# Performance work log

Measured on AMD Instinct MI355X. Metric: run time of the kernel, lower is better.

The kernel has to match this reference:

```python
import jax, jax.numpy as jnp
import numpy as np

DIM = 768
HEADS = 12
HEAD_DIM = DIM // HEADS
HIDDEN = 4 * DIM
EPS = 1e-5


def layernorm(x, g, b):
    mu = jnp.mean(x, axis=-1, keepdims=True)
    var = jnp.var(x, axis=-1, keepdims=True)
    return (x - mu) * jax.lax.rsqrt(var + EPS) * g + b


def setup_inputs() -> dict:
    key = jax.random.key(0)
    ks = jax.random.split(key, 16)
    s = 0.02
    return {
        "x_pre": jax.random.normal(ks[0], (8, 512, DIM), jnp.float32),
        "x_post": jax.random.normal(ks[1], (8, 512, DIM), jnp.float32),
        "attention_mask": jnp.zeros((8, 1, 1024, 1024), jnp.float32),
        "ln1_g": jnp.ones((DIM,), jnp.float32),
        "ln1_b": jnp.zeros((DIM,), jnp.float32),
        "Wq": jax.random.normal(ks[2], (DIM, DIM), jnp.float32) * s,
        "bq": jnp.zeros((DIM,), jnp.float32),
        "Wk": jax.random.normal(ks[3], (DIM, DIM), jnp.float32) * s,
        "bk": jnp.zeros((DIM,), jnp.float32),
        "Wv": jax.random.normal(ks[4], (DIM, DIM), jnp.float32) * s,
        "bv": jnp.zeros((DIM,), jnp.float32),
        "Wo": jax.random.normal(ks[5], (DIM, DIM), jnp.float32) * s,
        "bo": jnp.zeros((DIM,), jnp.float32),
        "ln2_g": jnp.ones((DIM,), jnp.float32),
        "ln2_b": jnp.zeros((DIM,), jnp.float32),
        "W1": jax.random.normal(ks[6], (DIM, HIDDEN), jnp.float32) * s,
        "b1": jnp.zeros((HIDDEN,), jnp.float32),
        "W2": jax.random.normal(ks[7], (HIDDEN, DIM), jnp.float32) * s,
        "b2": jnp.zeros((DIM,), jnp.float32),
        "gamma_1": 0.1 * jnp.ones((DIM,), jnp.float32),
        "gamma_2": 0.1 * jnp.ones((DIM,), jnp.float32),
    }


def reference(x_pre, x_post, attention_mask, ln1_g, ln1_b, Wq, bq, Wk, bk, Wv, bv,
              Wo, bo, ln2_g, ln2_b, W1, b1, W2, b2, gamma_1, gamma_2):
    x = jnp.concatenate((x_pre, x_post), axis=1)  # [B, N, C]
    B, N, C = x.shape
    h = layernorm(x, ln1_g, ln1_b)
    # self-attention with manual QK^T in float32
    q = (h @ Wq + bq).reshape(B, N, HEADS, HEAD_DIM)
    k = (h @ Wk + bk).reshape(B, N, HEADS, HEAD_DIM)
    v = (h @ Wv + bv).reshape(B, N, HEADS, HEAD_DIM)
    scale = HEAD_DIM ** -0.5
    attn = jnp.einsum("bqhd,bkhd->bhqk", q.astype(jnp.float32) * scale,
                      k.astype(jnp.float32)) + attention_mask
    attn = jax.nn.softmax(attn, axis=-1).astype(x.dtype)
    o = jnp.einsum("bhqk,bkhd->bqhd", attn, v).reshape(B, N, C)
    o = o @ Wo + bo
    x = x + gamma_1 * o
    # MLP
    h2 = layernorm(x, ln2_g, ln2_b)
    h2 = jax.nn.gelu(h2 @ W1 + b1, approximate=False) @ W2 + b2
    return x + gamma_2 * h2
```

## Files before the change

kernel.cpp:

```cpp
#include <hip/hip_runtime.h>
#include <hip/hip_fp8.h>
#include <cstdint>
#include <cstddef>

#define BATCH   8
#define SEQ     1024
#define DIMC    768
#define HEADS   12
#define HDIM    64
#define HIDDEN  3072
#define MROWS   (BATCH * SEQ)
#define L2E     1.4426950408889634f

typedef __attribute__((ext_vector_type(8))) short bf16x8;
typedef __attribute__((ext_vector_type(4))) float f32x4;

__device__ __forceinline__ unsigned short f2b(float f) {
    union { float f; unsigned int u; } v; v.f = f;
    unsigned int u = v.u;
    return (unsigned short)((u + 0x7FFFu + ((u >> 16) & 1u)) >> 16);
}
__device__ __forceinline__ unsigned char f2e4m3(float f) {
    __hip_fp8_e4m3 t(f); return t.__x;
}
__device__ __forceinline__ unsigned int b2u(float f) {
    union { float f; unsigned int u; } v; v.f = f; return v.u;
}
__device__ __forceinline__ float u2f(unsigned int u) {
    union { unsigned int u; float f; } v; v.u = u; return v.f;
}
__device__ __forceinline__ unsigned int pack2(float a, float b) {
    return ((b2u(a) + 0x8000u) >> 16) | (((b2u(b) + 0x8000u) & 0xFFFF0000u));
}
__device__ __forceinline__ void gl_lds16(const void* g, void* l) {
    __builtin_amdgcn_global_load_lds(
        (const __attribute__((address_space(1))) unsigned int*)g,
        (__attribute__((address_space(3))) unsigned int*)l, 16, 0, 0);
}
__device__ __forceinline__ float gelu_fast(float x) {
    float p = x * x;
    float a = fmaf(p, 0.044715f, 1.0f);
    float w = x * a * -2.302118131f;
    float z = exp2f(w);
    return x * __builtin_amdgcn_rcpf(1.0f + z);
}

__global__ __launch_bounds__(256) void tcvt_k(const float* __restrict__ src,
                                              unsigned char* __restrict__ dst,
                                              int K, int N) {
    __shared__ float tile[32][33];
    int k0 = blockIdx.y * 32, n0 = blockIdx.x * 32;
    int tx = threadIdx.x, ty = threadIdx.y;
#pragma unroll
    for (int i = 0; i < 4; i++)
        tile[ty + i * 8][tx] = src[(size_t)(k0 + ty + i * 8) * N + n0 + tx];
    __syncthreads();
#pragma unroll
    for (int i = 0; i < 4; i++)
        dst[(size_t)(n0 + ty + i * 8) * K + k0 + tx] = f2e4m3(tile[tx][ty + i * 8]);
}

__global__ __launch_bounds__(256) void tcvt4_k(const float* __restrict__ s0,
                                               const float* __restrict__ s1,
                                               const float* __restrict__ s2,
                                               const float* __restrict__ s3,
                                               unsigned char* __restrict__ d0,
                                               unsigned char* __restrict__ d1,
                                               unsigned char* __restrict__ d2,
                                               unsigned char* __restrict__ d3) {
    const float* src = (blockIdx.z == 0) ? s0 : (blockIdx.z == 1) ? s1
                     : (blockIdx.z == 2) ? s2 : s3;
    unsigned char* dst = (blockIdx.z == 0) ? d0 : (blockIdx.z == 1) ? d1
                       : (blockIdx.z == 2) ? d2 : d3;
    __shared__ float tile[32][33];
    int k0 = blockIdx.y * 32, n0 = blockIdx.x * 32;
    int tx = threadIdx.x, ty = threadIdx.y;
#pragma unroll
    for (int i = 0; i < 4; i++)
        tile[ty + i * 8][tx] = src[(size_t)(k0 + ty + i * 8) * DIMC + n0 + tx];
    __syncthreads();
#pragma unroll
    for (int i = 0; i < 4; i++)
        dst[(size_t)(n0 + ty + i * 8) * DIMC + k0 + tx] = f2e4m3(tile[tx][ty + i * 8]);
}

__global__ __launch_bounds__(256) void mprep_k(const float* __restrict__ m,
                                               unsigned short* __restrict__ mb) {
    size_t i = ((size_t)blockIdx.x * 256 + threadIdx.x) * 8;
    float4 a = *(const float4*)(m + i);
    float4 b = *(const float4*)(m + i + 4);
    uint4 o;
    o.x = pack2(a.x * L2E, a.y * L2E);
    o.y = pack2(a.z * L2E, a.w * L2E);
    o.z = pack2(b.x * L2E, b.y * L2E);
    o.w = pack2(b.z * L2E, b.w * L2E);
    *(uint4*)(mb + i) = o;
}

__global__ __launch_bounds__(256) void vtr_k(const unsigned short* __restrict__ src,
                                             unsigned char* __restrict__ dst) {
    int bh = blockIdx.x, k0 = blockIdx.y * 64;
    __shared__ unsigned short t[64][68];
    const unsigned short* s = src + ((size_t)bh * SEQ + k0) * HDIM;
    unsigned char* d = dst + (size_t)bh * HDIM * SEQ + k0;
    int tid = threadIdx.x;
#pragma unroll
    for (int p = 0; p < 4; p++) {
        int c = p * 256 + tid;
        int key = c >> 4, dd = (c & 15) * 4;
        *(uint2*)&t[key][dd] = *(const uint2*)&s[key * HDIM + dd];
    }
    __syncthreads();
#pragma unroll
    for (int p = 0; p < 8; p++) {
        int idx = p * 256 + tid;
        int dd = idx >> 5, kk = (idx & 31) * 2;
        uchar2 o;
        o.x = f2e4m3(u2f((unsigned int)t[kk][dd] << 16));
        o.y = f2e4m3(u2f((unsigned int)t[kk + 1][dd] << 16));
        *(uchar2*)&d[(size_t)dd * SEQ + kk] = o;
    }
}

__global__ __launch_bounds__(256) void ln_k(const float* __restrict__ xa,
                                            const float* __restrict__ xb,
                                            const float* __restrict__ g,
                                            const float* __restrict__ bt,
                                            float* __restrict__ x_out,
                                            unsigned char* __restrict__ h_out) {
    int r = blockIdx.x;
    const float* src;
    if (xb) {
        int b = r >> 10, nn = r & 1023;
        src = (nn < 512) ? xa + ((size_t)b * 512 + nn) * DIMC
                         : xb + ((size_t)b * 512 + (nn - 512)) * DIMC;
    } else {
        src = xa + (size_t)r * DIMC;
    }
    int t = threadIdx.x;
    float v[3], s = 0.f, s2 = 0.f;
#pragma unroll
    for (int j = 0; j < 3; j++) {
        v[j] = src[t + j * 256];
        s += v[j]; s2 += v[j] * v[j];
    }
#pragma unroll
    for (int off = 32; off > 0; off >>= 1) {
        s  += __shfl_down(s,  off);
        s2 += __shfl_down(s2, off);
    }
    __shared__ float red[8];
    int wid = t >> 6, lane = t & 63;
    if (lane == 0) { red[wid] = s; red[4 + wid] = s2; }
    __syncthreads();
    s  = red[0] + red[1] + red[2] + red[3];
    s2 = red[4] + red[5] + red[6] + red[7];
    float mu  = s * (1.f / DIMC);
    float var = s2 * (1.f / DIMC) - mu * mu;
    float rstd = rsqrtf(var + 1e-5f);
#pragma unroll
    for (int j = 0; j < 3; j++) {
        int i = t + j * 256;
        float xv = v[j];
        if (x_out) x_out[(size_t)r * DIMC + i] = xv;
        h_out[(size_t)r * DIMC + i] = f2e4m3((xv - mu) * rstd * g[i] + bt[i]);
    }
}

template <int MODE>
__global__ __launch_bounds__(256) void gemm_k(
    const unsigned char* __restrict__ A,
    const unsigned char* __restrict__ Bt0,
    const unsigned char* __restrict__ Bt1,
    const unsigned char* __restrict__ Bt2,
    const float* __restrict__ bias0,
    const float* __restrict__ bias1,
    const float* __restrict__ bias2,
    const float* __restrict__ resid,
    const float* __restrict__ gamma,
    float* __restrict__ outf,
    unsigned short* __restrict__ outb0,
    unsigned short* __restrict__ outb1,
    unsigned short* __restrict__ outb2,
    unsigned char* __restrict__ outc,
    int K, int ldo) {

    const int tid  = threadIdx.x;
    const int wid  = tid >> 6, lane = tid & 63;
    const int quad = lane >> 4, l16 = lane & 15;
    const int m0 = blockIdx.y * 128, n0 = blockIdx.x * 128;
    const int waveM = (wid >> 1) * 64, waveN = (wid & 1) * 64;

    const unsigned char* Bt = Bt0;
    if (MODE == 0) Bt = (blockIdx.z == 0) ? Bt0 : (blockIdx.z == 1) ? Bt1 : Bt2;

    __shared__ __align__(16) unsigned char As[128 * 128];
    __shared__ __align__(16) unsigned char Bs[128 * 128];

    int crow[4], coff[4];
#pragma unroll
    for (int j = 0; j < 4; j++) {
        int c = j * 256 + wid * 64 + lane;
        crow[j] = c >> 3;
        coff[j] = ((c & 7) ^ (crow[j] & 7)) * 16;
    }
    const int asw = l16 & 7;
    int abase[4], bbase[4];
#pragma unroll
    for (int i = 0; i < 4; i++) {
        abase[i] = (waveM + i * 16 + l16) * 128 + (quad & 1) * 8;
        bbase[i] = (waveN + i * 16 + l16) * 128 + (quad & 1) * 8;
    }

    f32x4 acc[4][4] = {};

    for (int k0 = 0; k0 < K; k0 += 128) {
#pragma unroll
        for (int j = 0; j < 4; j++)
            gl_lds16(&A[(size_t)(m0 + crow[j]) * K + k0 + coff[j]],
                     &As[(j * 256 + wid * 64) * 16]);
#pragma unroll
        for (int j = 0; j < 4; j++)
            gl_lds16(&Bt[(size_t)(n0 + crow[j]) * K + k0 + coff[j]],
                     &Bs[(j * 256 + wid * 64) * 16]);
        __syncthreads();

#pragma unroll
        for (int kk = 0; kk < 4; kk++) {
            const int csw = ((kk * 2 + (quad >> 1)) ^ asw) * 16;
            long a[4], b[4];
#pragma unroll
            for (int i = 0; i < 4; i++) a[i] = *(const long*)&As[abase[i] + csw];
#pragma unroll
            for (int i = 0; i < 4; i++) b[i] = *(const long*)&Bs[bbase[i] + csw];
#pragma unroll
            for (int i = 0; i < 4; i++)
#pragma unroll
                for (int j = 0; j < 4; j++)
                    acc[i][j] = __builtin_amdgcn_mfma_f32_16x16x32_fp8_fp8(
                        a[i], b[j], acc[i][j], 0, 0, 0);
        }
        __syncthreads();
    }

    const float* bias = bias0;
    unsigned short* outb = outb0;
    if (MODE == 0) {
        bias = (blockIdx.z == 0) ? bias0 : (blockIdx.z == 1) ? bias1 : bias2;
        outb = (blockIdx.z == 0) ? outb0 : (blockIdx.z == 1) ? outb1 : outb2;
    }
#pragma unroll
    for (int i = 0; i < 4; i++) {
#pragma unroll
        for (int j = 0; j < 4; j++) {
            int n = n0 + waveN + j * 16 + l16;
#pragma unroll
            for (int r = 0; r < 4; r++) {
                int m = m0 + waveM + i * 16 + quad * 4 + r;
                float val = acc[i][j][r];
                if (MODE == 0) {
                    val += bias[n];
                    int bb = m >> 10, nn = m & 1023;
                    int hh = n >> 6,  d  = n & 63;
                    outb[(((size_t)bb * HEADS + hh) * SEQ + nn) * HDIM + d] = f2b(val);
                } else if (MODE == 1 || MODE == 3) {
                    val += bias[n];
                    outf[(size_t)m * ldo + n] =
                        resid[(size_t)m * ldo + n] + gamma[n] * val;
                } else {
                    outc[(size_t)m * ldo + n] = f2e4m3(gelu_fast(val + bias[n]));
                }
            }
        }
    }
}

__global__ __launch_bounds__(256) void attn_k(const unsigned short* __restrict__ Q,
                                              const unsigned short* __restrict__ Km,
                                              const unsigned char* __restrict__ Vt,
                                              const unsigned short* __restrict__ maskb,
                                              unsigned char* __restrict__ O) {
    const int bh = blockIdx.x;
    const int b = bh / HEADS, h = bh - b * HEADS;
    const int tid = threadIdx.x;
    const int wid = tid >> 6, lane = tid & 63;
    const int quad = lane >> 4, l16 = lane & 15;
    const int qw = blockIdx.y * 64 + wid * 16;

    __shared__ __align__(16) unsigned short Ks[128 * 64];
    __shared__ __align__(16) unsigned char  Vs[64 * 128];
    __shared__ __align__(16) unsigned char  Ps[4][16 * 136];
    unsigned char* sp = Ps[wid];

    const unsigned short* Qp = Q + ((size_t)bh * SEQ + qw) * HDIM;
    bf16x8 aQ[2];
    aQ[0] = *(const bf16x8*)(Qp + l16 * HDIM + quad * 8);
    aQ[1] = *(const bf16x8*)(Qp + l16 * HDIM + 32 + quad * 8);

    int kql[4], vql[2];
#pragma unroll
    for (int j = 0; j < 4; j++) {
        int ck = (wid * 4 + j) * 64 + lane;
        int key = ck >> 3, ch = ck & 7;
        kql[j] = key * HDIM + ((ch ^ ((key >> 3) & 7)) * 8);
    }
#pragma unroll
    for (int j = 0; j < 2; j++) {
        int cv = j * 256 + wid * 64 + lane;
        int d = cv >> 3, ch = cv & 7;
        vql[j] = d * SEQ + ((ch ^ (d & 7)) * 16);
    }
    const unsigned short* Kb = Km + (size_t)bh * SEQ * HDIM;
    const unsigned char*  Vb = Vt + (size_t)bh * HDIM * SEQ;
    const unsigned short* Mbase = maskb + (size_t)b * SEQ * SEQ
                                + (size_t)(qw + quad * 4) * SEQ + 8 * l16;

    f32x4 o[4] = {};
    float lsum[4] = {};
    const float SCL2E = 0.125f * L2E;

    for (int key0 = 0; key0 < SEQ; key0 += 128) {
        float mreg[4][8];
#pragma unroll
        for (int r = 0; r < 4; r++) {
            uint4 w = *(const uint4*)(Mbase + key0 + r * SEQ);
            mreg[r][0] = u2f(w.x << 16); mreg[r][1] = u2f(w.x & 0xFFFF0000u);
            mreg[r][2] = u2f(w.y << 16); mreg[r][3] = u2f(w.y & 0xFFFF0000u);
            mreg[r][4] = u2f(w.z << 16); mreg[r][5] = u2f(w.z & 0xFFFF0000u);
            mreg[r][6] = u2f(w.w << 16); mreg[r][7] = u2f(w.w & 0xFFFF0000u);
        }
        const unsigned short* Kg = Kb + (size_t)key0 * HDIM;
        const unsigned char*  Vg = Vb + key0;
#pragma unroll
        for (int j = 0; j < 4; j++)
            gl_lds16(Kg + kql[j], &Ks[(wid * 4 + j) * 512]);
#pragma unroll
        for (int j = 0; j < 2; j++)
            gl_lds16(Vg + vql[j], &Vs[(j * 256 + wid * 64) * 16]);
        __syncthreads();

        f32x4 s[8];
#pragma unroll
        for (int nt = 0; nt < 8; nt++) {
            const unsigned short* kp = &Ks[(8 * l16 + nt) * 64];
            bf16x8 b0 = *(const bf16x8*)&kp[(quad ^ (l16 & 7)) * 8];
            bf16x8 b1 = *(const bf16x8*)&kp[((4 + quad) ^ (l16 & 7)) * 8];
            f32x4 t = {};
            t = __builtin_amdgcn_mfma_f32_16x16x32_bf16(aQ[0], b0, t, 0, 0, 0);
            t = __builtin_amdgcn_mfma_f32_16x16x32_bf16(aQ[1], b1, t, 0, 0, 0);
            s[nt] = t;
        }

#pragma unroll
        for (int r = 0; r < 4; r++) {
            float e[8];
#pragma unroll
            for (int nt = 0; nt < 8; nt++)
                e[nt] = exp2f(fmaf(s[nt][r], SCL2E, mreg[r][nt]));
            lsum[r] += ((e[0] + e[1]) + (e[2] + e[3])) +
                       ((e[4] + e[5]) + (e[6] + e[7]));
            unsigned int d0 = __builtin_amdgcn_cvt_pk_fp8_f32(e[0], e[1], 0, false);
            d0 = __builtin_amdgcn_cvt_pk_fp8_f32(e[2], e[3], d0, true);
            unsigned int d1 = __builtin_amdgcn_cvt_pk_fp8_f32(e[4], e[5], 0, false);
            d1 = __builtin_amdgcn_cvt_pk_fp8_f32(e[6], e[7], d1, true);
            int prow = quad * 4 + r;
            uint2 pv; pv.x = d0; pv.y = d1;
            *(uint2*)&sp[prow * 136 + ((l16 ^ (prow & 7)) * 8)] = pv;
        }
        __builtin_amdgcn_wave_barrier();

        long aP[4];
#pragma unroll
        for (int kt = 0; kt < 4; kt++)
            aP[kt] = *(const long*)&sp[l16 * 136 + (((kt * 4 + quad) ^ (l16 & 7)) * 8)];
#pragma unroll
        for (int dt = 0; dt < 4; dt++) {
            const unsigned char* vp = &Vs[(dt * 16 + l16) * 128];
            f32x4 oo = o[dt];
#pragma unroll
            for (int kt = 0; kt < 4; kt++) {
                long bv = *(const long*)
                    &vp[(((kt * 2 + (quad >> 1)) ^ (l16 & 7)) * 16) + (quad & 1) * 8];
                oo = __builtin_amdgcn_mfma_f32_16x16x32_fp8_fp8(aP[kt], bv, oo, 0, 0, 0);
            }
            o[dt] = oo;
        }
        __syncthreads();
    }

#pragma unroll
    for (int r = 0; r < 4; r++) {
        float v = lsum[r];
#pragma unroll
        for (int off = 8; off > 0; off >>= 1)
            v += __shfl_xor(v, off, 16);
        float inv = 1.0f / v;
#pragma unroll
        for (int dt = 0; dt < 4; dt++)
            O[(size_t)(b * SEQ + qw + quad * 4 + r) * DIMC + h * HDIM + dt * 16 + l16] =
                f2e4m3(o[dt][r] * inv);
    }
}

extern "C" void kernel_launch(void* const* d_in, const int* in_sizes, int n_in,
                              void* d_out, int out_size, void* d_ws, size_t ws_size,
                              hipStream_t stream) {
    const float* x_pre = (const float*)d_in[0];
    const float* x_post= (const float*)d_in[1];
    const float* mask  = (const float*)d_in[2];
    const float* ln1g  = (const float*)d_in[3];
    const float* ln1b  = (const float*)d_in[4];
    const float* Wq    = (const float*)d_in[5];
    const float* bq    = (const float*)d_in[6];
    const float* Wk    = (const float*)d_in[7];
    const float* bk    = (const float*)d_in[8];
    const float* Wv    = (const float*)d_in[9];
    const float* bv    = (const float*)d_in[10];
    const float* Wo    = (const float*)d_in[11];
    const float* bo    = (const float*)d_in[12];
    const float* ln2g  = (const float*)d_in[13];
    const float* ln2b  = (const float*)d_in[14];
    const float* W1    = (const float*)d_in[15];
    const float* b1    = (const float*)d_in[16];
    const float* W2    = (const float*)d_in[17];
    const float* b2    = (const float*)d_in[18];
    const float* g1    = (const float*)d_in[19];
    const float* g2    = (const float*)d_in[20];
    float* out = (float*)d_out;

    char* p = (char*)d_ws;
    float* xf  = (float*)p;                  p += (size_t)MROWS * DIMC * 4;
    float* x2f = (float*)p;                  p += (size_t)MROWS * DIMC * 4;
    unsigned char* h8  = (unsigned char*)p;  p += (size_t)MROWS * DIMC;
    unsigned char* O8  = (unsigned char*)p;  p += (size_t)MROWS * DIMC;
    unsigned char* G8  = (unsigned char*)p;  p += (size_t)MROWS * HIDDEN;
    unsigned short* Qb = (unsigned short*)p; p += (size_t)MROWS * DIMC * 2;
    unsigned short* Kb = (unsigned short*)p; p += (size_t)MROWS * DIMC * 2;
    unsigned short* Vb = (unsigned short*)p; p += (size_t)MROWS * DIMC * 2;
    unsigned char* V8  = (unsigned char*)p;  p += (size_t)MROWS * DIMC;
    unsigned short* Mb = (unsigned short*)p; p += (size_t)BATCH * SEQ * SEQ * 2;
    unsigned char* Wq8 = (unsigned char*)p;  p += (size_t)DIMC * DIMC;
    unsigned char* Wk8 = (unsigned char*)p;  p += (size_t)DIMC * DIMC;
    unsigned char* Wv8 = (unsigned char*)p;  p += (size_t)DIMC * DIMC;
    unsigned char* Wo8 = (unsigned char*)p;  p += (size_t)DIMC * DIMC;
    unsigned char* W18 = (unsigned char*)p;  p += (size_t)DIMC * HIDDEN;
    unsigned char* W28 = (unsigned char*)p;  p += (size_t)DIMC * HIDDEN;

    dim3 tb(32, 8);
    tcvt4_k<<<dim3(24, 24, 4), tb, 0, stream>>>(Wq, Wk, Wv, Wo, Wq8, Wk8, Wv8, Wo8);
    tcvt_k<<<dim3(96, 24), tb, 0, stream>>>(W1, W18, DIMC, HIDDEN);
    tcvt_k<<<dim3(24, 96), tb, 0, stream>>>(W2, W28, HIDDEN, DIMC);
    mprep_k<<<4096, 256, 0, stream>>>(mask, Mb);

    ln_k<<<MROWS, 256, 0, stream>>>(x_pre, x_post, ln1g, ln1b, xf, h8);

    gemm_k<0><<<dim3(6, 64, 3), 256, 0, stream>>>(h8, Wq8, Wk8, Wv8,
        bq, bk, bv, nullptr, nullptr, nullptr, Qb, Kb, Vb, nullptr, DIMC, DIMC);

    vtr_k<<<dim3(96, 16), 256, 0, stream>>>(Vb, V8);

    attn_k<<<dim3(96, 16), 256, 0, stream>>>(Qb, Kb, V8, Mb, O8);

    gemm_k<1><<<dim3(6, 64), 256, 0, stream>>>(O8, Wo8, nullptr, nullptr,
        bo, nullptr, nullptr, xf, g1, x2f, nullptr, nullptr, nullptr, nullptr, DIMC, DIMC);

    ln_k<<<MROWS, 256, 0, stream>>>(x2f, nullptr, ln2g, ln2b, nullptr, h8);

    gemm_k<2><<<dim3(24, 64), 256, 0, stream>>>(h8, W18, nullptr, nullptr,
        b1, nullptr, nullptr, nullptr, nullptr, nullptr, nullptr, nullptr, nullptr,
        G8, DIMC, HIDDEN);

    gemm_k<3><<<dim3(6, 64), 256, 0, stream>>>(G8, W28, nullptr, nullptr,
        b2, nullptr, nullptr, x2f, g2, out, nullptr, nullptr, nullptr, nullptr,
        HIDDEN, DIMC);

    (void)in_sizes; (void)n_in; (void)out_size; (void)ws_size;
}
```

Before: 393.4 us.

## Drop mask prep kernel, fold Q scale into GEMM, MFMA row sums, smaller M tiles

Removes the separate kernel that converted the fp32 mask to scaled bf16; attention now reads the fp32 mask directly and folds the log2e scaling into the exp argument. The softmax scale is applied to Q in the QKV GEMM epilogue. Softmax row sums are now computed by an MFMA against a ones vector on the fp8 probabilities rather than by scalar adds and shuffles, which also makes the denominator consistent with the quantized P. The GEMM gets a templated M tile, and the N=768 GEMMs use 64-row tiles for more blocks. The cost is doubled mask bytes read inside attention and extra MFMA work.

```diff
diff --git a/kernel.cpp b/kernel.cpp
--- a/kernel.cpp
+++ b/kernel.cpp
@@ -28,9 +28,6 @@
 }
 __device__ __forceinline__ float u2f(unsigned int u) {
     union { unsigned int u; float f; } v; v.u = u; return v.f;
-}
-__device__ __forceinline__ unsigned int pack2(float a, float b) {
-    return ((b2u(a) + 0x8000u) >> 16) | (((b2u(b) + 0x8000u) & 0xFFFF0000u));
 }
 __device__ __forceinline__ void gl_lds16(const void* g, void* l) {
     __builtin_amdgcn_global_load_lds(
@@ -84,19 +81,6 @@
         dst[(size_t)(n0 + ty + i * 8) * DIMC + k0 + tx] = f2e4m3(tile[tx][ty + i * 8]);
 }
 
-__global__ __launch_bounds__(256) void mprep_k(const float* __restrict__ m,
-                                               unsigned short* __restrict__ mb) {
-    size_t i = ((size_t)blockIdx.x * 256 + threadIdx.x) * 8;
-    float4 a = *(const float4*)(m + i);
-    float4 b = *(const float4*)(m + i + 4);
-    uint4 o;
-    o.x = pack2(a.x * L2E, a.y * L2E);
-    o.y = pack2(a.z * L2E, a.w * L2E);
-    o.z = pack2(b.x * L2E, b.y * L2E);
-    o.w = pack2(b.z * L2E, b.w * L2E);
-    *(uint4*)(mb + i) = o;
-}
-
 __global__ __launch_bounds__(256) void vtr_k(const unsigned short* __restrict__ src,
                                              unsigned char* __restrict__ dst) {
     int bh = blockIdx.x, k0 = blockIdx.y * 64;
@@ -167,7 +151,7 @@
     }
 }
 
-template <int MODE>
+template <int MODE, int TM>
 __global__ __launch_bounds__(256) void gemm_k(
     const unsigned char* __restrict__ A,
     const unsigned char* __restrict__ Bt0,
@@ -185,56 +169,64 @@
     unsigned char* __restrict__ outc,
     int K, int ldo) {
 
+    constexpr int AI = TM / 32;
     const int tid  = threadIdx.x;
     const int wid  = tid >> 6, lane = tid & 63;
     const int quad = lane >> 4, l16 = lane & 15;
-    const int m0 = blockIdx.y * 128, n0 = blockIdx.x * 128;
-    const int waveM = (wid >> 1) * 64, waveN = (wid & 1) * 64;
+    const int m0 = blockIdx.y * TM, n0 = blockIdx.x * 128;
+    const int waveM = (wid >> 1) * (AI * 16), waveN = (wid & 1) * 64;
 
     const unsigned char* Bt = Bt0;
     if (MODE == 0) Bt = (blockIdx.z == 0) ? Bt0 : (blockIdx.z == 1) ? Bt1 : Bt2;
 
-    __shared__ __align__(16) unsigned char As[128 * 128];
+    __shared__ __align__(16) unsigned char As[TM * 128];
     __shared__ __align__(16) unsigned char Bs[128 * 128];
 
-    int crow[4], coff[4];
+    int carow[AI], caoff[AI], cbrow[4], cboff[4];
+#pragma unroll
+    for (int j = 0; j < AI; j++) {
+        int c = j * 256 + tid;
+        carow[j] = c >> 3;
+        caoff[j] = ((c & 7) ^ (carow[j] & 7)) * 16;
+    }
 #pragma unroll
     for (int j = 0; j < 4; j++) {
-        int c = j * 256 + wid * 64 + lane;
-        crow[j] = c >> 3;
-        coff[j] = ((c & 7) ^ (crow[j] & 7)) * 16;
+        int c = j * 256 + tid;
+        cbrow[j] = c >> 3;
+        cboff[j] = ((c & 7) ^ (cbrow[j] & 7)) * 16;
     }
     const int asw = l16 & 7;
-    int abase[4], bbase[4];
-#pragma unroll
-    for (int i = 0; i < 4; i++) {
+    int abase[AI], bbase[4];
+#pragma unroll
+    for (int i = 0; i < AI; i++)
         abase[i] = (waveM + i * 16 + l16) * 128 + (quad & 1) * 8;
+#pragma unroll
+    for (int i = 0; i < 4; i++)
         bbase[i] = (waveN + i * 16 + l16) * 128 + (quad & 1) * 8;
-    }
-
-    f32x4 acc[4][4] = {};
+
+    f32x4 acc[AI][4] = {};
 
     for (int k0 = 0; k0 < K; k0 += 128) {
 #pragma unroll
+        for (int j = 0; j < AI; j++)
+            gl_lds16(&A[(size_t)(m0 + carow[j]) * K + k0 + caoff[j]],
+                     &As[(j * 256 + wid * 64) * 16]);
+#pragma unroll
         for (int j = 0; j < 4; j++)
-            gl_lds16(&A[(size_t)(m0 + crow[j]) * K + k0 + coff[j]],
-                     &As[(j * 256 + wid * 64) * 16]);
-#pragma unroll
-        for (int j = 0; j < 4; j++)
-            gl_lds16(&Bt[(size_t)(n0 + crow[j]) * K + k0 + coff[j]],
+            gl_lds16(&Bt[(size_t)(n0 + cbrow[j]) * K + k0 + cboff[j]],
                      &Bs[(j * 256 + wid * 64) * 16]);
         __syncthreads();
 
 #pragma unroll
         for (int kk = 0; kk < 4; kk++) {
             const int csw = ((kk * 2 + (quad >> 1)) ^ asw) * 16;
-            long a[4], b[4];
-#pragma unroll
-            for (int i = 0; i < 4; i++) a[i] = *(const long*)&As[abase[i] + csw];
+            long a[AI], b[4];
+#pragma unroll
+            for (int i = 0; i < AI; i++) a[i] = *(const long*)&As[abase[i] + csw];
 #pragma unroll
             for (int i = 0; i < 4; i++) b[i] = *(const long*)&Bs[bbase[i] + csw];
 #pragma unroll
-            for (int i = 0; i < 4; i++)
+            for (int i = 0; i < AI; i++)
 #pragma unroll
                 for (int j = 0; j < 4; j++)
                     acc[i][j] = __builtin_amdgcn_mfma_f32_16x16x32_fp8_fp8(
@@ -249,8 +241,9 @@
         bias = (blockIdx.z == 0) ? bias0 : (blockIdx.z == 1) ? bias1 : bias2;
         outb = (blockIdx.z == 0) ? outb0 : (blockIdx.z == 1) ? outb1 : outb2;
     }
-#pragma unroll
-    for (int i = 0; i < 4; i++) {
+    const float qscale = 0.125f * L2E;
+#pragma unroll
+    for (int i = 0; i < AI; i++) {
 #pragma unroll
         for (int j = 0; j < 4; j++) {
             int n = n0 + waveN + j * 16 + l16;
@@ -260,6 +253,7 @@
                 float val = acc[i][j][r];
                 if (MODE == 0) {
                     val += bias[n];
+                    if (blockIdx.z == 0) val *= qscale;
                     int bb = m >> 10, nn = m & 1023;
                     int hh = n >> 6,  d  = n & 63;
                     outb[(((size_t)bb * HEADS + hh) * SEQ + nn) * HDIM + d] = f2b(val);
@@ -278,7 +272,7 @@
 __global__ __launch_bounds__(256) void attn_k(const unsigned short* __restrict__ Q,
                                               const unsigned short* __restrict__ Km,
                                               const unsigned char* __restrict__ Vt,
-                                              const unsigned short* __restrict__ maskb,
+                                              const float* __restrict__ mask,
                                               unsigned char* __restrict__ O) {
     const int bh = blockIdx.x;
     const int b = bh / HEADS, h = bh - b * HEADS;
@@ -312,22 +306,22 @@
     }
     const unsigned short* Kb = Km + (size_t)bh * SEQ * HDIM;
     const unsigned char*  Vb = Vt + (size_t)bh * HDIM * SEQ;
-    const unsigned short* Mbase = maskb + (size_t)b * SEQ * SEQ
-                                + (size_t)(qw + quad * 4) * SEQ + 8 * l16;
+    const float* Mbase = mask + (size_t)b * SEQ * SEQ
+                       + (size_t)(qw + quad * 4) * SEQ + 8 * l16;
 
     f32x4 o[4] = {};
-    float lsum[4] = {};
-    const float SCL2E = 0.125f * L2E;
+    f32x4 osum = {};
+    const long ONES = 0x3838383838383838L;
 
     for (int key0 = 0; key0 < SEQ; key0 += 128) {
         float mreg[4][8];
+        const float* mb = Mbase + key0;
 #pragma unroll
         for (int r = 0; r < 4; r++) {
-            uint4 w = *(const uint4*)(Mbase + key0 + r * SEQ);
-            mreg[r][0] = u2f(w.x << 16); mreg[r][1] = u2f(w.x & 0xFFFF0000u);
-            mreg[r][2] = u2f(w.y << 16); mreg[r][3] = u2f(w.y & 0xFFFF0000u);
-            mreg[r][4] = u2f(w.z << 16); mreg[r][5] = u2f(w.z & 0xFFFF0000u);
-            mreg[r][6] = u2f(w.w << 16); mreg[r][7] = u2f(w.w & 0xFFFF0000u);
+            float4 u0 = *(const float4*)(mb + r * SEQ);
+            float4 u1 = *(const float4*)(mb + r * SEQ + 4);
+            mreg[r][0] = u0.x; mreg[r][1] = u0.y; mreg[r][2] = u0.z; mreg[r][3] = u0.w;
+            mreg[r][4] = u1.x; mreg[r][5] = u1.y; mreg[r][6] = u1.z; mreg[r][7] = u1.w;
         }
         const unsigned short* Kg = Kb + (size_t)key0 * HDIM;
         const unsigned char*  Vg = Vb + key0;
@@ -356,9 +350,7 @@
             float e[8];
 #pragma unroll
             for (int nt = 0; nt < 8; nt++)
-                e[nt] = exp2f(fmaf(s[nt][r], SCL2E, mreg[r][nt]));
-            lsum[r] += ((e[0] + e[1]) + (e[2] + e[3])) +
-                       ((e[4] + e[5]) + (e[6] + e[7]));
+                e[nt] = exp2f(fmaf(mreg[r][nt], L2E, s[nt][r]));
             unsigned int d0 = __builtin_amdgcn_cvt_pk_fp8_f32(e[0], e[1], 0, false);
             d0 = __builtin_amdgcn_cvt_pk_fp8_f32(e[2], e[3], d0, true);
             unsigned int d1 = __builtin_amdgcn_cvt_pk_fp8_f32(e[4], e[5], 0, false);
@@ -374,6 +366,9 @@
         for (int kt = 0; kt < 4; kt++)
             aP[kt] = *(const long*)&sp[l16 * 136 + (((kt * 4 + quad) ^ (l16 & 7)) * 8)];
 #pragma unroll
+        for (int kt = 0; kt < 4; kt++)
+            osum = __builtin_amdgcn_mfma_f32_16x16x32_fp8_fp8(aP[kt], ONES, osum, 0, 0, 0);
+#pragma unroll
         for (int dt = 0; dt < 4; dt++) {
             const unsigned char* vp = &Vs[(dt * 16 + l16) * 128];
             f32x4 oo = o[dt];
@@ -390,11 +385,7 @@
 
 #pragma unroll
     for (int r = 0; r < 4; r++) {
-        float v = lsum[r];
-#pragma unroll
-        for (int off = 8; off > 0; off >>= 1)
-            v += __shfl_xor(v, off, 16);
-        float inv = 1.0f / v;
+        float inv = 1.0f / osum[r];
 #pragma unroll
         for (int dt = 0; dt < 4; dt++)
             O[(size_t)(b * SEQ + qw + quad * 4 + r) * DIMC + h * HDIM + dt * 16 + l16] =
@@ -438,7 +429,6 @@
     unsigned short* Kb = (unsigned short*)p; p += (size_t)MROWS * DIMC * 2;
     unsigned short* Vb = (unsigned short*)p; p += (size_t)MROWS * DIMC * 2;
     unsigned char* V8  = (unsigned char*)p;  p += (size_t)MROWS * DIMC;
-    unsigned short* Mb = (unsigned short*)p; p += (size_t)BATCH * SEQ * SEQ * 2;
     unsigned char* Wq8 = (unsigned char*)p;  p += (size_t)DIMC * DIMC;
     unsigned char* Wk8 = (unsigned char*)p;  p += (size_t)DIMC * DIMC;
     unsigned char* Wv8 = (unsigned char*)p;  p += (size_t)DIMC * DIMC;
@@ -450,27 +440,26 @@
     tcvt4_k<<<dim3(24, 24, 4), tb, 0, stream>>>(Wq, Wk, Wv, Wo, Wq8, Wk8, Wv8, Wo8);
     tcvt_k<<<dim3(96, 24), tb, 0, stream>>>(W1, W18, DIMC, HIDDEN);
     tcvt_k<<<dim3(24, 96), tb, 0, stream>>>(W2, W28, HIDDEN, DIMC);
-    mprep_k<<<4096, 256, 0, stream>>>(mask, Mb);
 
     ln_k<<<MROWS, 256, 0, stream>>>(x_pre, x_post, ln1g, ln1b, xf, h8);
 
-    gemm_k<0><<<dim3(6, 64, 3), 256, 0, stream>>>(h8, Wq8, Wk8, Wv8,
+    gemm_k<0, 128><<<dim3(6, 64, 3), 256, 0, stream>>>(h8, Wq8, Wk8, Wv8,
         bq, bk, bv, nullptr, nullptr, nullptr, Qb, Kb, Vb, nullptr, DIMC, DIMC);
 
     vtr_k<<<dim3(96, 16), 256, 0, stream>>>(Vb, V8);
 
-    attn_k<<<dim3(96, 16), 256, 0, stream>>>(Qb, Kb, V8, Mb, O8);
-
-    gemm_k<1><<<dim3(6, 64), 256, 0, stream>>>(O8, Wo8, nullptr, nullptr,
+    attn_k<<<dim3(96, 16), 256, 0, stream>>>(Qb, Kb, V8, mask, O8);
+
+    gemm_k<1, 64><<<dim3(6, 128), 256, 0, stream>>>(O8, Wo8, nullptr, nullptr,
         bo, nullptr, nullptr, xf, g1, x2f, nullptr, nullptr, nullptr, nullptr, DIMC, DIMC);
 
     ln_k<<<MROWS, 256, 0, stream>>>(x2f, nullptr, ln2g, ln2b, nullptr, h8);
 
-    gemm_k<2><<<dim3(24, 64), 256, 0, stream>>>(h8, W18, nullptr, nullptr,
+    gemm_k<2, 128><<<dim3(24, 64), 256, 0, stream>>>(h8, W18, nullptr, nullptr,
         b1, nullptr, nullptr, nullptr, nullptr, nullptr, nullptr, nullptr, nullptr,
         G8, DIMC, HIDDEN);
 
-    gemm_k<3><<<dim3(6, 64), 256, 0, stream>>>(G8, W28, nullptr, nullptr,
+    gemm_k<3, 64><<<dim3(6, 128), 256, 0, stream>>>(G8, W28, nullptr, nullptr,
         b2, nullptr, nullptr, x2f, g2, out, nullptr, nullptr, nullptr, nullptr,
         HIDDEN, DIMC);
 
```

Measured after the change: 380.0 us. 3.4% less time.
